# Kernel optimization log

Hardware: AMD Instinct MI355X
Metric: run time of the kernel (lower is better)

The kernel has to match this reference:

```python
import jax, jax.numpy as jnp
import numpy as np
import math

H = 4            # cross_attn_heads
SPARSE_RATIO = 0.6
B, N, C = 128, 196, 768


def setup_inputs() -> dict:
    key = jax.random.key(0)
    ks = jax.random.split(key, 10)
    xav = (6.0 / (C + C)) ** 0.5  # xavier_uniform bound for square Linear
    inp = {
        "RGB_cash": jax.random.normal(ks[0], (B, N, C), jnp.float32),
        "NI_cash": jax.random.normal(ks[1], (B, N, C), jnp.float32),
        "TI_cash": jax.random.normal(ks[2], (B, N, C), jnp.float32),
        "RGB_global": jax.random.normal(ks[3], (B, C), jnp.float32),
        "NI_global": jax.random.normal(ks[4], (B, C), jnp.float32),
        "TI_global": jax.random.normal(ks[5], (B, C), jnp.float32),
        # 9 CrossModalAttention modules, stacked: q_proj / k_proj weights (out,in) and biases
        "q_w": jax.random.uniform(ks[6], (9, C, C), jnp.float32, -xav, xav),
        "q_b": jnp.zeros((9, C), jnp.float32),
        "k_w": jax.random.uniform(ks[7], (9, C, C), jnp.float32, -xav, xav),
        "k_b": jnp.zeros((9, C), jnp.float32),
        # 3 TokenSparse modal_weights, init torch.ones(3); small noise for non-degenerate softmax
        "modal_w": jnp.ones((3, 3), jnp.float32) + 0.01 * jax.random.normal(ks[8], (3, 3), jnp.float32),
    }
    return inp


def _cos_sim(patches, g):
    # patches (B,N,C), g (B,C) -> (B,N); F.normalize eps=1e-12
    pn = patches / jnp.maximum(jnp.linalg.norm(patches, axis=-1, keepdims=True), 1e-12)
    gn = g / jnp.maximum(jnp.linalg.norm(g, axis=-1, keepdims=True), 1e-12)
    return jnp.einsum("bnc,bc->bn", pn, gn)


def _cross_attn(patches, g, cos, qw, qb, kw, kb):
    # CrossModalAttention.forward: Q from global (1 token), K from patches, softmax over N
    b, n, c = patches.shape
    d = c // H
    q = (g @ qw.T + qb).reshape(b, H, d)              # (B,H,D)
    k = (patches @ kw.T + kb).reshape(b, n, H, d)     # (B,N,H,D)
    attn = jnp.einsum("bhd,bnhd->bhn", q, k) * (d ** -0.5)
    attn = jax.nn.softmax(attn, axis=-1)              # (B,H,N)
    return (attn * cos[:, None, :]).mean(axis=1)      # (B,N)


def _minmax(s):
    smin = s.min(axis=-1, keepdims=True)
    smax = s.max(axis=-1, keepdims=True)
    return (s - smin) / (smax - smin + 1e-8)


def _token_sparse(tokens, s_im, s_m2, s_m3, mw):
    b, n, c = tokens.shape
    w = jax.nn.softmax(mw)
    score = w[0] * _minmax(s_im) + w[1] * _minmax(s_m2) + w[2] * _minmax(s_m3)
    num_keep = max(1, math.ceil(n * SPARSE_RATIO))
    _, idx = jax.lax.top_k(score, num_keep)           # == descending sort, first num_keep
    mask = jnp.zeros((b, n), score.dtype).at[jnp.arange(b)[:, None], idx].set(1.0)
    return tokens * mask[..., None], mask


def reference(RGB_cash, NI_cash, TI_cash, RGB_global, NI_global, TI_global,
              q_w, q_b, k_w, k_b, modal_w):
    toks = [RGB_cash, NI_cash, TI_cash]
    glbs = [RGB_global, NI_global, TI_global]
    # module order: rgb_self, rgb_x_nir, rgb_x_tir, nir_self, nir_x_rgb, nir_x_tir,
    #               tir_self, tir_x_rgb, tir_x_nir
    order = [(0, 0), (0, 1), (0, 2), (1, 1), (1, 0), (1, 2), (2, 2), (2, 0), (2, 1)]
    scores = []
    for i, (pi, gi) in enumerate(order):
        cos = _cos_sim(toks[pi], glbs[gi])
        scores.append(_cross_attn(toks[pi], glbs[gi], cos, q_w[i], q_b[i], k_w[i], k_b[i]))
    out_rgb, m_rgb = _token_sparse(RGB_cash, scores[0], scores[1], scores[2], modal_w[0])
    out_nir, m_nir = _token_sparse(NI_cash, scores[3], scores[4], scores[5], modal_w[1])
    out_tir, m_tir = _token_sparse(TI_cash, scores[6], scores[7], scores[8], modal_w[2])
    return (out_rgb, out_nir, out_tir, m_rgb, m_nir, m_tir)
```

## Files before the change

### kernel.cpp

```cpp
#include <hip/hip_runtime.h>
#include <math.h>

#define BB   128
#define NN   196
#define CC   768
#define HH   4
#define DD   192
#define TOK_PER   19267584
#define NROWS_ALL 75264
#define NUM_KEEP  118
#define SCALE_D   0.07216878364870322f

#define OFF_QPART 0
#define SZ_QPART  (2*9*128*768)
#define OFF_VV    (OFF_QPART + SZ_QPART)
#define SZ_VV     (9*128*4*768)

__device__ __forceinline__ float4 f4fma(float s, float4 b, float4 a) {
  a.x = fmaf(s, b.x, a.x); a.y = fmaf(s, b.y, a.y);
  a.z = fmaf(s, b.z, a.z); a.w = fmaf(s, b.w, a.w);
  return a;
}
__device__ __forceinline__ float f4dot(float4 p, float4 q) {
  return p.x*q.x + p.y*q.y + p.z*q.z + p.w*q.w;
}

__global__ __launch_bounds__(256) void k_qproj(const float* __restrict__ g0,
                                               const float* __restrict__ g1,
                                               const float* __restrict__ g2,
                                               const float* __restrict__ qw,
                                               float* __restrict__ qpart) {
  __shared__ __align__(16) float AsT[32 * 68];
  __shared__ __align__(16) float WsT[32 * 68];
  const int gtab[9] = {0, 1, 2, 1, 0, 2, 2, 0, 1};
  int i = blockIdx.y, z = blockIdx.z;
  int mt = blockIdx.x & 1, nt = blockIdx.x >> 1;
  int tid = threadIdx.x, tx = tid & 15, ty = tid >> 4;
  int gi = gtab[i];
  const float4* A4 = (const float4*)((gi == 0) ? g0 : ((gi == 1) ? g1 : g2));
  const float4* W4 = (const float4*)(qw + (size_t)i * CC * CC);
  float4 acc0 = {0,0,0,0}, acc1 = {0,0,0,0}, acc2 = {0,0,0,0}, acc3 = {0,0,0,0};
  int arow = mt * 64, wrow = nt * 64;
  int kb4 = z * 96;
  for (int kk = 0; kk < 12; kk++) {
    #pragma unroll
    for (int f = tid; f < 512; f += 256) {
      int r = f >> 3, k4 = f & 7;
      float4 va = A4[(size_t)(arow + r) * 192 + kb4 + kk * 8 + k4];
      float4 vw = W4[(size_t)(wrow + r) * 192 + kb4 + kk * 8 + k4];
      int kq = 4 * k4;
      AsT[(kq+0)*68 + r] = va.x; AsT[(kq+1)*68 + r] = va.y;
      AsT[(kq+2)*68 + r] = va.z; AsT[(kq+3)*68 + r] = va.w;
      WsT[(kq+0)*68 + r] = vw.x; WsT[(kq+1)*68 + r] = vw.y;
      WsT[(kq+2)*68 + r] = vw.z; WsT[(kq+3)*68 + r] = vw.w;
    }
    __syncthreads();
    #pragma unroll
    for (int k = 0; k < 32; k++) {
      float4 a = *(const float4*)&AsT[k * 68 + 4 * ty];
      float4 w = *(const float4*)&WsT[k * 68 + 4 * tx];
      acc0 = f4fma(a.x, w, acc0); acc1 = f4fma(a.y, w, acc1);
      acc2 = f4fma(a.z, w, acc2); acc3 = f4fma(a.w, w, acc3);
    }
    __syncthreads();
  }
  float* dst = qpart + (size_t)(z * 9 + i) * 128 * CC;
  int col = wrow + 4 * tx;
  int row = arow + 4 * ty;
  *(float4*)&dst[(size_t)(row + 0) * CC + col] = acc0;
  *(float4*)&dst[(size_t)(row + 1) * CC + col] = acc1;
  *(float4*)&dst[(size_t)(row + 2) * CC + col] = acc2;
  *(float4*)&dst[(size_t)(row + 3) * CC + col] = acc3;
}

__global__ __launch_bounds__(256) void k_vvproj(const float* __restrict__ qpart,
                                                const float* __restrict__ qb,
                                                const float* __restrict__ kw,
                                                float* __restrict__ vvout) {
  __shared__ __align__(16) float AsT[32 * 68];
  __shared__ __align__(16) float Bs[32 * 68];
  int ih = blockIdx.y; int i = ih >> 2, h = ih & 3;
  int mt = blockIdx.x & 1, nt = blockIdx.x >> 1;
  int tid = threadIdx.x, tx = tid & 15, ty = tid >> 4;
  const float4* qp0 = (const float4*)qpart + (size_t)i * 128 * 192;
  const float4* qp1 = (const float4*)qpart + (size_t)(9 + i) * 128 * 192;
  const float4* qb4 = (const float4*)qb + (size_t)i * 192;
  const float4* B4  = (const float4*)(kw + (size_t)i * CC * CC);
  float4 acc0 = {0,0,0,0}, acc1 = {0,0,0,0}, acc2 = {0,0,0,0}, acc3 = {0,0,0,0};
  int arow = mt * 64;
  int bcol4 = nt * 16;
  for (int kk = 0; kk < 6; kk++) {
    #pragma unroll
    for (int f = tid; f < 512; f += 256) {
      int r = f >> 3, k4 = f & 7;
      int colf4 = h * 48 + kk * 8 + k4;
      float4 va = qp0[(size_t)(arow + r) * 192 + colf4];
      float4 vb = qp1[(size_t)(arow + r) * 192 + colf4];
      float4 vq = qb4[colf4];
      va.x += vb.x + vq.x; va.y += vb.y + vq.y;
      va.z += vb.z + vq.z; va.w += vb.w + vq.w;
      int kq = 4 * k4;
      AsT[(kq+0)*68 + r] = va.x; AsT[(kq+1)*68 + r] = va.y;
      AsT[(kq+2)*68 + r] = va.z; AsT[(kq+3)*68 + r] = va.w;
      int rk = f >> 4, c4 = f & 15;
      float4 vB = B4[(size_t)(h * DD + kk * 32 + rk) * 192 + bcol4 + c4];
      *(float4*)&Bs[rk * 68 + 4 * c4] = vB;
    }
    __syncthreads();
    #pragma unroll
    for (int k = 0; k < 32; k++) {
      float4 a = *(const float4*)&AsT[k * 68 + 4 * ty];
      float4 bb = *(const float4*)&Bs[k * 68 + 4 * tx];
      acc0 = f4fma(a.x, bb, acc0); acc1 = f4fma(a.y, bb, acc1);
      acc2 = f4fma(a.z, bb, acc2); acc3 = f4fma(a.w, bb, acc3);
    }
    __syncthreads();
  }
  int col = nt * 64 + 4 * tx;
  int b0 = arow + 4 * ty;
  *(float4*)&vvout[((size_t)(i * 128 + b0 + 0) * 4 + h) * CC + col] = acc0;
  *(float4*)&vvout[((size_t)(i * 128 + b0 + 1) * 4 + h) * CC + col] = acc1;
  *(float4*)&vvout[((size_t)(i * 128 + b0 + 2) * 4 + h) * CC + col] = acc2;
  *(float4*)&vvout[((size_t)(i * 128 + b0 + 3) * 4 + h) * CC + col] = acc3;
}

__global__ __launch_bounds__(256, 2) void k_fused(const float* __restrict__ rgb,
                                                  const float* __restrict__ ni,
                                                  const float* __restrict__ ti,
                                                  const float* __restrict__ vv,
                                                  const float* __restrict__ g0,
                                                  const float* __restrict__ g1,
                                                  const float* __restrict__ g2,
                                                  const float* __restrict__ qpart,
                                                  const float* __restrict__ qb,
                                                  const float* __restrict__ kb,
                                                  const float* __restrict__ modal_w,
                                                  float* __restrict__ out,
                                                  float* __restrict__ outmask) {
  __shared__ float red[4][64 * 17];
  __shared__ __align__(16) float GN[3 * CC];
  __shared__ float SC[196 * 17];
  __shared__ float BIASs[12];
  __shared__ float CSUM[12];
  __shared__ float SV[3][196];
  __shared__ float MN[3], MX[3];
  __shared__ float sfinal[196];
  __shared__ float keepf[196];

  int bid = blockIdx.x;
  int t = bid >> 7;
  int b = bid & 127;
  int tid = threadIdx.x;
  int w = tid >> 6, lane = tid & 63;
  const float* toks = (t == 0) ? rgb : ((t == 1) ? ni : ti);
  int gi0, gi1, gi2;
  if (t == 0)      { gi0 = 0; gi1 = 1; gi2 = 2; }
  else if (t == 1) { gi0 = 1; gi1 = 0; gi2 = 2; }
  else             { gi0 = 2; gi1 = 0; gi2 = 1; }

  float4 V[36];
  #pragma unroll
  for (int k = 0; k < 3; k++) {
    #pragma unroll
    for (int h = 0; h < 4; h++) {
      const float4* src = (const float4*)(vv + (((size_t)(3*t + k) * 128 + b) * 4 + h) * CC);
      int v = k * 4 + h;
      V[3*v + 0] = src[lane];
      V[3*v + 1] = src[lane + 64];
      V[3*v + 2] = src[lane + 128];
    }
  }

  if (w < 3) {
    int gidx = (w == 0) ? gi0 : ((w == 1) ? gi1 : gi2);
    const float* gsrc = (gidx == 0) ? g0 : ((gidx == 1) ? g1 : g2);
    const float4* s4 = (const float4*)(gsrc + (size_t)b * CC);
    float4 u0 = s4[lane], u1 = s4[lane + 64], u2 = s4[lane + 128];
    float ss = f4dot(u0, u0) + f4dot(u1, u1) + f4dot(u2, u2);
    #pragma unroll
    for (int off = 32; off; off >>= 1) ss += __shfl_xor(ss, off);
    float inv = 1.0f / fmaxf(sqrtf(ss), 1e-12f);
    u0.x *= inv; u0.y *= inv; u0.z *= inv; u0.w *= inv;
    u1.x *= inv; u1.y *= inv; u1.z *= inv; u1.w *= inv;
    u2.x *= inv; u2.y *= inv; u2.z *= inv; u2.w *= inv;
    float4* d4 = (float4*)&GN[w * CC];
    d4[lane] = u0; d4[lane + 64] = u1; d4[lane + 128] = u2;

    int i = 3 * t + w;
    const float* qbb = qb + (size_t)i * CC;
    const float* kbb = kb + (size_t)i * CC;
    const float* q0p = qpart + ((size_t)i * 128 + b) * CC;
    const float* q1p = qpart + ((size_t)(9 + i) * 128 + b) * CC;
    #pragma unroll
    for (int h = 0; h < 4; h++) {
      int j0 = h * DD + lane;
      float s = (q0p[j0]       + q1p[j0]       + qbb[j0])       * kbb[j0]
              + (q0p[j0 + 64]  + q1p[j0 + 64]  + qbb[j0 + 64])  * kbb[j0 + 64]
              + (q0p[j0 + 128] + q1p[j0 + 128] + qbb[j0 + 128]) * kbb[j0 + 128];
      #pragma unroll
      for (int off = 32; off; off >>= 1) s += __shfl_xor(s, off);
      if (lane == 0) BIASs[w * 4 + h] = s;
    }
  }
  __syncthreads();

  int a_id = lane & 15;
  float bias_r = (a_id < 12) ? BIASs[a_id] : 0.f;

  float* myred = red[w];
  const float4* G4 = (const float4*)GN;
  int s_grp = lane >> 4;

  const float4* pr0 = (const float4*)(toks + ((size_t)b * NN + w) * CC);
  float4 pc0 = pr0[lane], pc1 = pr0[lane + 64], pc2 = pr0[lane + 128];

  for (int it = 0; it < 49; it++) {
    int row = it * 4 + w;

    int rn = row + 4;
    float4 pn0 = pc0, pn1 = pc1, pn2 = pc2;
    if (rn < NN) {
      const float4* pr = (const float4*)(toks + ((size_t)b * NN + rn) * CC);
      pn0 = pr[lane]; pn1 = pr[lane + 64]; pn2 = pr[lane + 128];
    }

    float a[16];
    #pragma unroll
    for (int v = 0; v < 12; v++)
      a[v] = f4dot(pc0, V[3*v]) + f4dot(pc1, V[3*v + 1]) + f4dot(pc2, V[3*v + 2]);
    #pragma unroll
    for (int j = 0; j < 3; j++)
      a[12 + j] = f4dot(pc0, G4[j*192 + lane])
                + f4dot(pc1, G4[j*192 + lane + 64])
                + f4dot(pc2, G4[j*192 + lane + 128]);
    a[15] = f4dot(pc0, pc0) + f4dot(pc1, pc1) + f4dot(pc2, pc2);

    #pragma unroll
    for (int v = 0; v < 16; v++) myred[lane * 17 + v] = a[v];
    __builtin_amdgcn_s_waitcnt(0xc07f);
    __builtin_amdgcn_sched_barrier(0);
    float part = 0.f;
    #pragma unroll
    for (int i2 = 0; i2 < 16; i2++)
      part += myred[(s_grp * 16 + i2) * 17 + a_id];
    part += __shfl_xor(part, 16, 64);
    part += __shfl_xor(part, 32, 64);

    float s15  = __shfl(part, 15, 64);
    float invp = 1.0f / fmaxf(sqrtf(s15), 1e-12f);
    float res;
    if (a_id < 12)      res = (part + bias_r) * SCALE_D;
    else if (a_id < 15) res = part * invp;
    else                res = invp;

    if (lane < 16) SC[row * 17 + lane] = res;
    pc0 = pn0; pc1 = pn1; pc2 = pn2;
  }
  __syncthreads();

  bool act = tid < NN;
  for (int c = w; c < 12; c += 4) {
    int n3 = lane + 192;
    float v0 = SC[(lane      ) * 17 + c];
    float v1 = SC[(lane +  64) * 17 + c];
    float v2 = SC[(lane + 128) * 17 + c];
    float v3 = (n3 < NN) ? SC[n3 * 17 + c] : -3.4e38f;
    float mx = fmaxf(fmaxf(v0, v1), fmaxf(v2, v3));
    #pragma unroll
    for (int off = 32; off; off >>= 1) mx = fmaxf(mx, __shfl_xor(mx, off));
    float e0 = expf(v0 - mx), e1 = expf(v1 - mx), e2 = expf(v2 - mx);
    float e3 = (n3 < NN) ? expf(v3 - mx) : 0.f;
    float es = e0 + e1 + e2 + e3;
    #pragma unroll
    for (int off = 32; off; off >>= 1) es += __shfl_xor(es, off);
    SC[(lane      ) * 17 + c] = e0;
    SC[(lane +  64) * 17 + c] = e1;
    SC[(lane + 128) * 17 + c] = e2;
    if (n3 < NN) SC[n3 * 17 + c] = e3;
    if (lane == 0) CSUM[c] = es;
  }
  __syncthreads();

  float scv0 = 0.f, scv1 = 0.f, scv2 = 0.f;
  if (act) {
    const float* r = &SC[tid * 17];
    float as0 = r[0]/CSUM[0] + r[1]/CSUM[1] + r[2]/CSUM[2]  + r[3]/CSUM[3];
    float as1 = r[4]/CSUM[4] + r[5]/CSUM[5] + r[6]/CSUM[6]  + r[7]/CSUM[7];
    float as2 = r[8]/CSUM[8] + r[9]/CSUM[9] + r[10]/CSUM[10] + r[11]/CSUM[11];
    scv0 = r[12] * as0 * 0.25f;
    scv1 = r[13] * as1 * 0.25f;
    scv2 = r[14] * as2 * 0.25f;
    SV[0][tid] = scv0; SV[1][tid] = scv1; SV[2][tid] = scv2;
  }
  __syncthreads();

  if (w < 3) {
    float u0 = SV[w][lane], u1 = SV[w][lane + 64], u2 = SV[w][lane + 128];
    float mn = fminf(fminf(u0, u1), u2);
    float mx = fmaxf(fmaxf(u0, u1), u2);
    if (lane + 192 < NN) {
      float u3 = SV[w][lane + 192];
      mn = fminf(mn, u3); mx = fmaxf(mx, u3);
    }
    #pragma unroll
    for (int off = 32; off; off >>= 1) {
      mn = fminf(mn, __shfl_xor(mn, off));
      mx = fmaxf(mx, __shfl_xor(mx, off));
    }
    if (lane == 0) { MN[w] = mn; MX[w] = mx; }
  }
  __syncthreads();

  float w0 = modal_w[t * 3 + 0], w1 = modal_w[t * 3 + 1], w2 = modal_w[t * 3 + 2];
  float wm = fmaxf(w0, fmaxf(w1, w2));
  float ew0 = expf(w0 - wm), ew1 = expf(w1 - wm), ew2 = expf(w2 - wm);
  float esum = ew0 + ew1 + ew2;
  float fv = 0.f;
  if (act) {
    fv = (ew0 / esum) * (scv0 - MN[0]) / (MX[0] - MN[0] + 1e-8f)
       + (ew1 / esum) * (scv1 - MN[1]) / (MX[1] - MN[1] + 1e-8f)
       + (ew2 / esum) * (scv2 - MN[2]) / (MX[2] - MN[2] + 1e-8f);
    sfinal[tid] = fv;
  }
  __syncthreads();

  if (act) {
    int cnt = 0;
    for (int j = 0; j < NN; j++) {
      float fj = sfinal[j];
      cnt += (fj > fv) || (fj == fv && j < tid);
    }
    float kf = (cnt < NUM_KEEP) ? 1.0f : 0.0f;
    keepf[tid] = kf;
    outmask[((size_t)t * 128 + b) * NN + tid] = kf;
  }
  __syncthreads();

  float* obase = out + ((size_t)t * 128 + b) * NN * CC;
  for (int r = w; r < NN; r += 4) {
    float4 o0 = {0,0,0,0}, o1 = {0,0,0,0}, o2 = {0,0,0,0};
    if (keepf[r] != 0.0f) {
      const float4* srcr = (const float4*)(toks + ((size_t)b * NN + r) * CC);
      o0 = srcr[lane]; o1 = srcr[lane + 64]; o2 = srcr[lane + 128];
    }
    float4* dstr = (float4*)(obase + (size_t)r * CC);
    dstr[lane] = o0; dstr[lane + 64] = o1; dstr[lane + 128] = o2;
  }
}

extern "C" void kernel_launch(void* const* d_in, const int* in_sizes, int n_in,
                              void* d_out, int out_size, void* d_ws, size_t ws_size,
                              hipStream_t stream) {
  const float* rgb = (const float*)d_in[0];
  const float* ni  = (const float*)d_in[1];
  const float* ti  = (const float*)d_in[2];
  const float* g0  = (const float*)d_in[3];
  const float* g1  = (const float*)d_in[4];
  const float* g2  = (const float*)d_in[5];
  const float* qw  = (const float*)d_in[6];
  const float* qb  = (const float*)d_in[7];
  const float* kw  = (const float*)d_in[8];
  const float* kb  = (const float*)d_in[9];
  const float* mw  = (const float*)d_in[10];

  float* ws    = (float*)d_ws;
  float* qpart = ws + OFF_QPART;
  float* vv    = ws + OFF_VV;
  float* outf  = (float*)d_out;
  float* maskb = outf + (size_t)3 * TOK_PER;

  k_qproj<<<dim3(24, 9, 2), 256, 0, stream>>>(g0, g1, g2, qw, qpart);
  k_vvproj<<<dim3(24, 36), 256, 0, stream>>>(qpart, qb, kw, vv);
  k_fused<<<384, 256, 0, stream>>>(rgb, ni, ti, vv, g0, g1, g2,
                                   qpart, qb, kb, mw, outf, maskb);
}
```

Baseline: 525.9 us.

## Split fused kernel into dot-score and mask kernels; copy tokens during streaming pass

The single fused kernel is split in two. The first kernel processes half a batch's rows per block, which doubles the grid to 768 blocks. It writes per-row scores to a workspace and copies every token row to the output while that row is already in registers. A second small kernel computes softmax, min-max normalisation and top-k ranking from the workspace scores, then zeroes only the dropped rows. This removes the second read of the token tensor in the final output pass and improves parallelism, at the cost of an extra launch, a score round-trip through global memory, and writing the dropped rows twice.

New measurement: 526.8 us. Within noise of the previous version (+0.2%).

```diff
diff --git a/kernel.cpp b/kernel.cpp
--- a/kernel.cpp
+++ b/kernel.cpp
@@ -7,7 +7,6 @@
 #define HH   4
 #define DD   192
 #define TOK_PER   19267584
-#define NROWS_ALL 75264
 #define NUM_KEEP  118
 #define SCALE_D   0.07216878364870322f
 
@@ -15,6 +14,8 @@
 #define SZ_QPART  (2*9*128*768)
 #define OFF_VV    (OFF_QPART + SZ_QPART)
 #define SZ_VV     (9*128*4*768)
+#define OFF_SC    (OFF_VV + SZ_VV)
+#define SZ_SC     (3*128*196*16)
 
 __device__ __forceinline__ float4 f4fma(float s, float4 b, float4 a) {
   a.x = fmaf(s, b.x, a.x); a.y = fmaf(s, b.y, a.y);
@@ -124,32 +125,25 @@
   *(float4*)&vvout[((size_t)(i * 128 + b0 + 3) * 4 + h) * CC + col] = acc3;
 }
 
-__global__ __launch_bounds__(256, 2) void k_fused(const float* __restrict__ rgb,
-                                                  const float* __restrict__ ni,
-                                                  const float* __restrict__ ti,
-                                                  const float* __restrict__ vv,
-                                                  const float* __restrict__ g0,
-                                                  const float* __restrict__ g1,
-                                                  const float* __restrict__ g2,
-                                                  const float* __restrict__ qpart,
-                                                  const float* __restrict__ qb,
-                                                  const float* __restrict__ kb,
-                                                  const float* __restrict__ modal_w,
-                                                  float* __restrict__ out,
-                                                  float* __restrict__ outmask) {
+__global__ __launch_bounds__(256, 2) void k_dots(const float* __restrict__ rgb,
+                                                 const float* __restrict__ ni,
+                                                 const float* __restrict__ ti,
+                                                 const float* __restrict__ vv,
+                                                 const float* __restrict__ g0,
+                                                 const float* __restrict__ g1,
+                                                 const float* __restrict__ g2,
+                                                 const float* __restrict__ qpart,
+                                                 const float* __restrict__ qb,
+                                                 const float* __restrict__ kb,
+                                                 float* __restrict__ sc,
+                                                 float* __restrict__ out) {
   __shared__ float red[4][64 * 17];
   __shared__ __align__(16) float GN[3 * CC];
-  __shared__ float SC[196 * 17];
   __shared__ float BIASs[12];
-  __shared__ float CSUM[12];
-  __shared__ float SV[3][196];
-  __shared__ float MN[3], MX[3];
-  __shared__ float sfinal[196];
-  __shared__ float keepf[196];
-
   int bid = blockIdx.x;
-  int t = bid >> 7;
-  int b = bid & 127;
+  int t = bid >> 8;
+  int rem = bid & 255;
+  int b = rem >> 1, half = rem & 1;
   int tid = threadIdx.x;
   int w = tid >> 6, lane = tid & 63;
   const float* toks = (t == 0) ? rgb : ((t == 1) ? ni : ti);
@@ -210,17 +204,21 @@
   float* myred = red[w];
   const float4* G4 = (const float4*)GN;
   int s_grp = lane >> 4;
-
-  const float4* pr0 = (const float4*)(toks + ((size_t)b * NN + w) * CC);
+  int n0 = half * 98;
+  float* obase = out + ((size_t)t * 128 + b) * NN * CC;
+
+  const float4* pr0 = (const float4*)(toks + ((size_t)b * NN + n0 + w) * CC);
   float4 pc0 = pr0[lane], pc1 = pr0[lane + 64], pc2 = pr0[lane + 128];
 
-  for (int it = 0; it < 49; it++) {
-    int row = it * 4 + w;
-
-    int rn = row + 4;
+  for (int it = 0; it < 25; it++) {
+    int row_local = it * 4 + w;
+    if (row_local >= 98) break;
+    int n = n0 + row_local;
+
+    int rl_next = row_local + 4;
     float4 pn0 = pc0, pn1 = pc1, pn2 = pc2;
-    if (rn < NN) {
-      const float4* pr = (const float4*)(toks + ((size_t)b * NN + rn) * CC);
+    if (rl_next < 98) {
+      const float4* pr = (const float4*)(toks + ((size_t)b * NN + n0 + rl_next) * CC);
       pn0 = pr[lane]; pn1 = pr[lane + 64]; pn2 = pr[lane + 128];
     }
 
@@ -234,6 +232,11 @@
                 + f4dot(pc1, G4[j*192 + lane + 64])
                 + f4dot(pc2, G4[j*192 + lane + 128]);
     a[15] = f4dot(pc0, pc0) + f4dot(pc1, pc1) + f4dot(pc2, pc2);
+
+    {
+      float4* dstr = (float4*)(obase + (size_t)n * CC);
+      dstr[lane] = pc0; dstr[lane + 64] = pc1; dstr[lane + 128] = pc2;
+    }
 
     #pragma unroll
     for (int v = 0; v < 16; v++) myred[lane * 17 + v] = a[v];
@@ -253,18 +256,47 @@
     else if (a_id < 15) res = part * invp;
     else                res = invp;
 
-    if (lane < 16) SC[row * 17 + lane] = res;
+    if (lane < 16) {
+      float* scrow = sc + (((size_t)t * 128 + b) * 196 + n) * 16;
+      scrow[lane] = res;
+    }
     pc0 = pn0; pc1 = pn1; pc2 = pn2;
   }
-  __syncthreads();
-
+}
+
+__global__ __launch_bounds__(256) void k_mask(const float* __restrict__ sc,
+                                              const float* __restrict__ modal_w,
+                                              float* __restrict__ out,
+                                              float* __restrict__ outmask) {
+  __shared__ float S[196 * 17];
+  __shared__ float CSUM[12];
+  __shared__ float SV[3][196];
+  __shared__ float MN[3], MX[3];
+  __shared__ float sfinal[196];
+  __shared__ float keepf[196];
+  int b = blockIdx.x, m = blockIdx.y;
+  int tid = threadIdx.x;
+  int w = tid >> 6, lane = tid & 63;
   bool act = tid < NN;
+
+  const float4* base = (const float4*)(sc + ((size_t)m * 128 + b) * 196 * 16);
+  if (act) {
+    float4 r0 = base[tid*4+0], r1 = base[tid*4+1], r2 = base[tid*4+2], r3 = base[tid*4+3];
+    float* d = &S[tid * 17];
+    d[0] = r0.x; d[1] = r0.y; d[2]  = r0.z; d[3]  = r0.w;
+    d[4] = r1.x; d[5] = r1.y; d[6]  = r1.z; d[7]  = r1.w;
+    d[8] = r2.x; d[9] = r2.y; d[10] = r2.z; d[11] = r2.w;
+    d[12] = r3.x; d[13] = r3.y; d[14] = r3.z;
+  }
+  __syncthreads();
+
+  #pragma unroll
   for (int c = w; c < 12; c += 4) {
     int n3 = lane + 192;
-    float v0 = SC[(lane      ) * 17 + c];
-    float v1 = SC[(lane +  64) * 17 + c];
-    float v2 = SC[(lane + 128) * 17 + c];
-    float v3 = (n3 < NN) ? SC[n3 * 17 + c] : -3.4e38f;
+    float v0 = S[(lane      ) * 17 + c];
+    float v1 = S[(lane +  64) * 17 + c];
+    float v2 = S[(lane + 128) * 17 + c];
+    float v3 = (n3 < NN) ? S[n3 * 17 + c] : -3.4e38f;
     float mx = fmaxf(fmaxf(v0, v1), fmaxf(v2, v3));
     #pragma unroll
     for (int off = 32; off; off >>= 1) mx = fmaxf(mx, __shfl_xor(mx, off));
@@ -273,17 +305,17 @@
     float es = e0 + e1 + e2 + e3;
     #pragma unroll
     for (int off = 32; off; off >>= 1) es += __shfl_xor(es, off);
-    SC[(lane      ) * 17 + c] = e0;
-    SC[(lane +  64) * 17 + c] = e1;
-    SC[(lane + 128) * 17 + c] = e2;
-    if (n3 < NN) SC[n3 * 17 + c] = e3;
+    S[(lane      ) * 17 + c] = e0;
+    S[(lane +  64) * 17 + c] = e1;
+    S[(lane + 128) * 17 + c] = e2;
+    if (n3 < NN) S[n3 * 17 + c] = e3;
     if (lane == 0) CSUM[c] = es;
   }
   __syncthreads();
 
   float scv0 = 0.f, scv1 = 0.f, scv2 = 0.f;
   if (act) {
-    const float* r = &SC[tid * 17];
+    const float* r = &S[tid * 17];
     float as0 = r[0]/CSUM[0] + r[1]/CSUM[1] + r[2]/CSUM[2]  + r[3]/CSUM[3];
     float as1 = r[4]/CSUM[4] + r[5]/CSUM[5] + r[6]/CSUM[6]  + r[7]/CSUM[7];
     float as2 = r[8]/CSUM[8] + r[9]/CSUM[9] + r[10]/CSUM[10] + r[11]/CSUM[11];
@@ -311,7 +343,7 @@
   }
   __syncthreads();
 
-  float w0 = modal_w[t * 3 + 0], w1 = modal_w[t * 3 + 1], w2 = modal_w[t * 3 + 2];
+  float w0 = modal_w[m * 3 + 0], w1 = modal_w[m * 3 + 1], w2 = modal_w[m * 3 + 2];
   float wm = fmaxf(w0, fmaxf(w1, w2));
   float ew0 = expf(w0 - wm), ew1 = expf(w1 - wm), ew2 = expf(w2 - wm);
   float esum = ew0 + ew1 + ew2;
@@ -332,19 +364,17 @@
     }
     float kf = (cnt < NUM_KEEP) ? 1.0f : 0.0f;
     keepf[tid] = kf;
-    outmask[((size_t)t * 128 + b) * NN + tid] = kf;
-  }
-  __syncthreads();
-
-  float* obase = out + ((size_t)t * 128 + b) * NN * CC;
+    outmask[((size_t)m * 128 + b) * NN + tid] = kf;
+  }
+  __syncthreads();
+
+  float* obase = out + ((size_t)m * 128 + b) * NN * CC;
+  float4 z = {0.f, 0.f, 0.f, 0.f};
   for (int r = w; r < NN; r += 4) {
-    float4 o0 = {0,0,0,0}, o1 = {0,0,0,0}, o2 = {0,0,0,0};
-    if (keepf[r] != 0.0f) {
-      const float4* srcr = (const float4*)(toks + ((size_t)b * NN + r) * CC);
-      o0 = srcr[lane]; o1 = srcr[lane + 64]; o2 = srcr[lane + 128];
-    }
-    float4* dstr = (float4*)(obase + (size_t)r * CC);
-    dstr[lane] = o0; dstr[lane + 64] = o1; dstr[lane + 128] = o2;
+    if (keepf[r] == 0.0f) {
+      float4* dstr = (float4*)(obase + (size_t)r * CC);
+      dstr[lane] = z; dstr[lane + 64] = z; dstr[lane + 128] = z;
+    }
   }
 }
 
@@ -366,11 +396,13 @@
   float* ws    = (float*)d_ws;
   float* qpart = ws + OFF_QPART;
   float* vv    = ws + OFF_VV;
+  float* sc    = ws + OFF_SC;
   float* outf  = (float*)d_out;
   float* maskb = outf + (size_t)3 * TOK_PER;
 
   k_qproj<<<dim3(24, 9, 2), 256, 0, stream>>>(g0, g1, g2, qw, qpart);
   k_vvproj<<<dim3(24, 36), 256, 0, stream>>>(qpart, qb, kw, vv);
-  k_fused<<<384, 256, 0, stream>>>(rgb, ni, ti, vv, g0, g1, g2,
-                                   qpart, qb, kb, mw, outf, maskb);
-}
+  k_dots<<<768, 256, 0, stream>>>(rgb, ni, ti, vv, g0, g1, g2,
+                                  qpart, qb, kb, sc, outf);
+  k_mask<<<dim3(128, 3), 256, 0, stream>>>(sc, mw, outf, maskb);
+}
```
